# Performance work log

Hardware: AMD Instinct MI355X
Metric: run time of the kernel (lower is better)

Reference implementation:

```python
import jax, jax.numpy as jnp
import numpy as np

B, CIN, H, W = 4, 1024, 64, 64
PLANES = 256
K = 3
DIL = 2
PAD = DIL * (K - 1) // 2  # = 2
EPS = 1e-5


def setup_inputs() -> dict:
    key = jax.random.key(0)
    ks = jax.random.split(key, 16)
    d = {}
    d['x'] = jax.random.normal(ks[0], (B, CIN, H, W), dtype=jnp.float32)
    # conv1: 1x1, inplanes->planes, no bias
    d['w1'] = jax.random.normal(ks[1], (PLANES, CIN), dtype=jnp.float32) * 0.02
    d['gamma1'] = jnp.ones((PLANES,), jnp.float32)
    d['beta1'] = jnp.zeros((PLANES,), jnp.float32)
    d['mean1'] = jax.random.normal(ks[2], (PLANES,), dtype=jnp.float32) * 0.1
    d['var1'] = jax.random.uniform(ks[3], (PLANES,), minval=0.5, maxval=1.5, dtype=jnp.float32)
    # deform_offset: 3x3 conv planes->18, with bias
    d['woff'] = jax.random.normal(ks[4], (18, PLANES, K, K), dtype=jnp.float32) * 0.01
    d['boff'] = jnp.zeros((18,), jnp.float32)
    # conv2 (deformable): 3x3 planes->planes, with bias
    d['w2'] = jax.random.normal(ks[5], (PLANES, PLANES, K, K), dtype=jnp.float32) * 0.02
    d['bconv2'] = jnp.zeros((PLANES,), jnp.float32)
    d['gamma2'] = jnp.ones((PLANES,), jnp.float32)
    d['beta2'] = jnp.zeros((PLANES,), jnp.float32)
    d['mean2'] = jax.random.normal(ks[6], (PLANES,), dtype=jnp.float32) * 0.1
    d['var2'] = jax.random.uniform(ks[7], (PLANES,), minval=0.5, maxval=1.5, dtype=jnp.float32)
    # conv3: 1x1 planes->planes*4, no bias
    d['w3'] = jax.random.normal(ks[8], (PLANES * 4, PLANES), dtype=jnp.float32) * 0.02
    d['gamma3'] = jnp.ones((PLANES * 4,), jnp.float32)
    d['beta3'] = jnp.zeros((PLANES * 4,), jnp.float32)
    d['mean3'] = jax.random.normal(ks[9], (PLANES * 4,), dtype=jnp.float32) * 0.1
    d['var3'] = jax.random.uniform(ks[10], (PLANES * 4,), minval=0.5, maxval=1.5, dtype=jnp.float32)
    return d


def _bn(x, gamma, beta, mean, var):
    # inference-mode BatchNorm over channel dim (NCHW)
    inv = jax.lax.rsqrt(var + EPS)
    return (x - mean[:, None, None]) * (inv * gamma)[:, None, None] + beta[:, None, None]


def _deform_conv(x, offset, w, b):
    # x: [B,C,H,W]; offset: [B,18,H,W] ordered (dy,dx) per kernel tap; w: [O,C,3,3]
    Bn, C, Hh, Ww = x.shape
    off = offset.reshape(Bn, K * K, 2, Hh, Ww)
    off_y, off_x = off[:, :, 0], off[:, :, 1]          # [B,9,H,W]
    kk = jnp.arange(K * K)
    base_y = (kk // K) * DIL - PAD                      # [9]
    base_x = (kk % K) * DIL - PAD
    ys = jnp.arange(Hh, dtype=x.dtype)
    xs = jnp.arange(Ww, dtype=x.dtype)
    py = base_y.astype(x.dtype)[None, :, None, None] + ys[None, None, :, None] + off_y
    px = base_x.astype(x.dtype)[None, :, None, None] + xs[None, None, None, :] + off_x

    def sample_one(img, py1, px1):
        # img [C,H,W]; py1/px1 [9,H,W] -> [C,9,H,W] bilinear with zero padding
        y0 = jnp.floor(py1)
        x0 = jnp.floor(px1)
        wy = py1 - y0
        wx = px1 - x0

        def gather(yc, xc):
            yi = yc.astype(jnp.int32)
            xi = xc.astype(jnp.int32)
            valid = ((yi >= 0) & (yi < Hh) & (xi >= 0) & (xi < Ww)).astype(img.dtype)
            yi = jnp.clip(yi, 0, Hh - 1)
            xi = jnp.clip(xi, 0, Ww - 1)
            return img[:, yi, xi] * valid[None]

        v00 = gather(y0, x0)
        v01 = gather(y0, x0 + 1)
        v10 = gather(y0 + 1, x0)
        v11 = gather(y0 + 1, x0 + 1)
        return (v00 * ((1 - wy) * (1 - wx))[None] + v01 * ((1 - wy) * wx)[None]
                + v10 * (wy * (1 - wx))[None] + v11 * (wy * wx)[None])

    sampled = jax.vmap(sample_one)(x, py, px)           # [B,C,9,H,W]
    out = jnp.einsum('bckhw,ock->bohw', sampled, w.reshape(w.shape[0], C, K * K))
    return out + b[None, :, None, None]


def reference(x, w1, gamma1, beta1, mean1, var1, woff, boff, w2, bconv2,
              gamma2, beta2, mean2, var2, w3, gamma3, beta3, mean3, var3):
    residual = x
    out = jnp.einsum('bchw,oc->bohw', x, w1)            # conv1 1x1
    out = jax.nn.relu(_bn(out, gamma1, beta1, mean1, var1))
    offset = jax.lax.conv_general_dilated(
        out, woff, window_strides=(1, 1), padding=((PAD, PAD), (PAD, PAD)),
        rhs_dilation=(DIL, DIL), dimension_numbers=('NCHW', 'OIHW', 'NCHW'))
    offset = offset + boff[None, :, None, None]
    out = _deform_conv(out, offset, w2, bconv2)
    out = jax.nn.relu(_bn(out, gamma2, beta2, mean2, var2))
    out = jnp.einsum('bchw,oc->bohw', out, w3)          # conv3 1x1
    out = _bn(out, gamma3, beta3, mean3, var3)
    return jax.nn.relu(out + residual)
```

## Files before the change

kernel.cpp:

```cpp
#include <hip/hip_runtime.h>

#define EPS_BN 1e-5f

typedef __bf16 bf16x8 __attribute__((ext_vector_type(8)));
typedef float f32x4 __attribute__((ext_vector_type(4)));

__device__ __forceinline__ unsigned short f2bf(float f) {
  union { float f; unsigned u; } v; v.f = f;
  unsigned r = v.u + 0x7fffu + ((v.u >> 16) & 1u);
  return (unsigned short)(r >> 16);
}
__device__ __forceinline__ float bf2f(unsigned short h) {
  union { unsigned u; float f; } v; v.u = ((unsigned)h) << 16;
  return v.f;
}

__global__ __launch_bounds__(256) void prep_all(
    const float* __restrict__ w1, const float* __restrict__ w2, const float* __restrict__ woff,
    const float* __restrict__ w3,
    const float* g1, const float* b1, const float* m1, const float* v1,
    const float* g2, const float* b2, const float* m2, const float* v2, const float* bconv2,
    const float* g3, const float* b3, const float* m3, const float* v3,
    unsigned short* __restrict__ w1b, unsigned short* __restrict__ w2r,
    uint4* __restrict__ act1Pz, unsigned short* __restrict__ wob,
    unsigned short* __restrict__ w3b, float* __restrict__ shift3,
    float* s1, float* h1, float* s2, float* h2) {
  int bid = blockIdx.x, tid = threadIdx.x;
  if (bid < 1024) {
    int i = bid * 256 + tid;
    w1b[i] = f2bf(w1[i]);
  } else if (bid < 3328) {
    int i = (bid - 1024) * 256 + tid;
    int o = i / 2304, r = i % 2304;
    int kk = r / 256, c = r % 256;
    w2r[i] = f2bf(w2[(size_t)o * 2304 + c * 9 + kk]);
  } else if (bid < 3592) {
    int i = (bid - 3328) * 256 + tid;
    int cell = i >> 5, q = i & 31;
    int b = cell / 528, r = cell - b * 528;
    int row, col;
    if (r < 136) { row = r / 68; col = r % 68; }
    else if (r < 272) { int rr = r - 136; row = 66 + rr / 68; col = rr % 68; }
    else { int rr = r - 272; row = 2 + (rr >> 2); int c4 = rr & 3; col = (c4 < 2) ? c4 : c4 + 64; }
    act1Pz[(((size_t)(b * 68) + row) * 68 + col) * 32 + q] = uint4{0, 0, 0, 0};
  } else if (bid < 3880) {
    int i = (bid - 3592) * 256 + tid;
    int o = i / 2304, r = i % 2304;
    int kk = r / 256, c = r % 256;
    wob[i] = (o < 18) ? f2bf(woff[(size_t)o * 2304 + c * 9 + kk]) : (unsigned short)0;
  } else if (bid < 4904) {
    int i = (bid - 3880) * 256 + tid;
    int o = i >> 8;
    float sc = rsqrtf(v3[o] + EPS_BN) * g3[o];
    w3b[i] = f2bf(w3[i] * sc);
  } else if (bid < 4908) {
    int c = (bid - 4904) * 256 + tid;
    float sc = rsqrtf(v3[c] + EPS_BN) * g3[c];
    shift3[c] = b3[c] - m3[c] * sc;
  } else {
    int c = tid;
    float sc1 = rsqrtf(v1[c] + EPS_BN) * g1[c];
    s1[c] = sc1; h1[c] = b1[c] - m1[c] * sc1;
    float sc2 = rsqrtf(v2[c] + EPS_BN) * g2[c];
    s2[c] = sc2; h2[c] = b2[c] + (bconv2[c] - m2[c]) * sc2;
  }
}

__global__ __launch_bounds__(256) void gemm1_x(
    const float* __restrict__ x, const unsigned short* __restrict__ Bm,
    unsigned short* __restrict__ part, int KH) {
  __shared__ __align__(16) char blob[16896];
  __shared__ __align__(16) unsigned short sA1[4096];
  __shared__ __align__(16) unsigned short sB1[4096];
  unsigned short* sA0 = (unsigned short*)blob;
  unsigned short* sB0 = (unsigned short*)(blob + 8192);
  float* tbuf = (float*)blob;
  int tid = threadIdx.x, lane = tid & 63, wv = tid >> 6;
  int z = blockIdx.z;
  int m0 = blockIdx.y * 128, n0 = blockIdx.x * 128;
  f32x4 acc[4][4] = {};
  int rowB = tid >> 2;
  int kcolBs = (((tid & 3) ^ (rowB & 3))) * 8;
  int px = tid & 127, chalf = tid >> 7;
  int s0w = (chalf * 2) ^ (px & 3), s1w = (chalf * 2 + 1) ^ (px & 3);
  int bb = m0 >> 12, p0 = m0 & 4095;
  const float* xa = x + (size_t)bb * 4194304 + (size_t)(chalf * 16) * 4096 + (p0 + px);
  int wm = wv & 1, wn = wv >> 1;
  int lane15 = lane & 15, quad = lane >> 4, l3 = lane & 3;

  float va[16];

#define G1_ISSUE_A(K0)                                                                    \
  {                                                                                       \
    const float* xp = xa + (size_t)(K0) * 4096;                                           \
    _Pragma("unroll") for (int j = 0; j < 16; ++j) va[j] = xp[(size_t)j * 4096];          \
  }

#define G1_ISSUE_B(DB, K0)                                                                \
  {                                                                                       \
    _Pragma("unroll") for (int r = 0; r < 2; ++r) {                                       \
      const unsigned short* gp = Bm + (size_t)(n0 + r * 64 + rowB) * 1024 + (K0) + kcolBs;\
      __builtin_amdgcn_global_load_lds((const __attribute__((address_space(1))) void*)gp, \
          (__attribute__((address_space(3))) void*)&(DB)[r * 2048 + wv * 512], 16, 0, 0); \
    }                                                                                     \
  }

#define G1_CVT_WRITE(DA)                                                                  \
  {                                                                                       \
    unsigned o8[8];                                                                       \
    _Pragma("unroll") for (int j = 0; j < 8; ++j)                                         \
      o8[j] = (unsigned)f2bf(va[2 * j]) | ((unsigned)f2bf(va[2 * j + 1]) << 16);          \
    *(uint4*)((DA) + px * 32 + s0w * 8) = uint4{o8[0], o8[1], o8[2], o8[3]};              \
    *(uint4*)((DA) + px * 32 + s1w * 8) = uint4{o8[4], o8[5], o8[6], o8[7]};              \
  }

#define G1_COMPUTE(DA, DB)                                                                \
  {                                                                                       \
    bf16x8 afr[4], bfr[4];                                                                \
    _Pragma("unroll") for (int mi = 0; mi < 4; ++mi)                                      \
      afr[mi] = *(const bf16x8*)&(DA)[(wm * 64 + mi * 16 + lane15) * 32 + (quad ^ l3) * 8]; \
    _Pragma("unroll") for (int ni = 0; ni < 4; ++ni)                                      \
      bfr[ni] = *(const bf16x8*)&(DB)[(wn * 64 + ni * 16 + lane15) * 32 + (quad ^ l3) * 8]; \
    _Pragma("unroll") for (int mi = 0; mi < 4; ++mi)                                      \
      _Pragma("unroll") for (int ni = 0; ni < 4; ++ni)                                    \
        acc[mi][ni] =                                                                     \
            __builtin_amdgcn_mfma_f32_16x16x32_bf16(afr[mi], bfr[ni], acc[mi][ni], 0, 0, 0); \
  }

#define G1_BODY(K0, AC, BC, AN, BN_)                                                      \
  {                                                                                       \
    G1_ISSUE_A(K0);                                                                       \
    G1_ISSUE_B(BN_, K0);                                                                  \
    asm volatile("s_waitcnt vmcnt(18)" ::: "memory");                                     \
    asm volatile("s_waitcnt lgkmcnt(0)" ::: "memory");                                    \
    __builtin_amdgcn_s_barrier();                                                         \
    G1_COMPUTE(AC, BC);                                                                   \
    asm volatile("s_waitcnt vmcnt(2)" ::: "memory");                                      \
    G1_CVT_WRITE(AN);                                                                     \
    __builtin_amdgcn_s_barrier();                                                         \
  }

  int kbase = z * KH;
  int nst = KH >> 5;
  G1_ISSUE_A(kbase);
  G1_ISSUE_B(sB0, kbase);
  asm volatile("s_waitcnt vmcnt(2)" ::: "memory");
  G1_CVT_WRITE(sA0);
  for (int t = 0; t + 2 < nst; t += 2) {
    G1_BODY(kbase + (t + 1) * 32, sA0, sB0, sA1, sB1);
    G1_BODY(kbase + (t + 2) * 32, sA1, sB1, sA0, sB0);
  }
  G1_BODY(kbase + (nst - 1) * 32, sA0, sB0, sA1, sB1);
  asm volatile("s_waitcnt vmcnt(0)" ::: "memory");
  asm volatile("s_waitcnt lgkmcnt(0)" ::: "memory");
  __builtin_amdgcn_s_barrier();
  G1_COMPUTE(sA1, sB1);
#undef G1_ISSUE_A
#undef G1_ISSUE_B
#undef G1_CVT_WRITE
#undef G1_COMPUTE
#undef G1_BODY

  unsigned short* outH = part + (size_t)z * 16384 * 256;
  int trow = tid >> 3;
  int tcol16 = (tid & 7) * 16;
  int growBase = m0 + (trow >> 4) * 64 + (trow & 15);
#pragma unroll
  for (int mi = 0; mi < 4; ++mi) {
    __syncthreads();
#pragma unroll
    for (int ni = 0; ni < 4; ++ni)
#pragma unroll
      for (int reg = 0; reg < 4; ++reg)
        tbuf[(wm * 16 + quad * 4 + reg) * 132 + wn * 64 + ni * 16 + lane15] = acc[mi][ni][reg];
    __syncthreads();
    int gr = growBase + mi * 16;
    const float* lp = &tbuf[trow * 132 + tcol16];
    unsigned o[8];
#pragma unroll
    for (int j = 0; j < 8; ++j)
      o[j] = (unsigned)f2bf(lp[2 * j]) | ((unsigned)f2bf(lp[2 * j + 1]) << 16);
    unsigned short* op = outH + (size_t)gr * 256 + n0 + tcol16;
    *(uint4*)(op) = uint4{o[0], o[1], o[2], o[3]};
    *(uint4*)(op + 8) = uint4{o[4], o[5], o[6], o[7]};
  }
}

__global__ __launch_bounds__(256) void gemm_split(
    const unsigned short* __restrict__ A, const unsigned short* __restrict__ Bm,
    unsigned short* __restrict__ part, int M, int N, int K, int KH) {
  __shared__ __align__(16) char blob[32768];
  __shared__ __align__(16) unsigned short sA1[8192];
  __shared__ __align__(16) unsigned short sB1[8192];
  unsigned short* sA0 = (unsigned short*)blob;
  unsigned short* sB0 = (unsigned short*)(blob + 16384);
  float* tbuf = (float*)blob;
  int tid = threadIdx.x, lane = tid & 63, wv = tid >> 6;
  int z = blockIdx.z;
  int m0 = blockIdx.y * 128, n0 = blockIdx.x * 128;
  f32x4 acc[4][4] = {};
  int rowS = tid >> 3;
  int colS = (((tid & 7) ^ (rowS & 7))) * 8;
  int wm = wv & 1, wn = wv >> 1;
  int lane15 = lane & 15, quad = lane >> 4, l7 = lane & 7;

#define GS_STAGE(dA, dB, K0)                                                              \
  {                                                                                       \
    int k0_ = (K0);                                                                       \
    _Pragma("unroll") for (int r = 0; r < 4; ++r) {                                       \
      const unsigned short* gp = A + (size_t)(m0 + r * 32 + rowS) * K + k0_ + colS;       \
      __builtin_amdgcn_global_load_lds((const __attribute__((address_space(1))) void*)gp, \
          (__attribute__((address_space(3))) void*)&(dA)[r * 2048 + wv * 512], 16, 0, 0); \
    }                                                                                     \
    _Pragma("unroll") for (int r = 0; r < 4; ++r) {                                       \
      const unsigned short* gp = Bm + (size_t)(n0 + r * 32 + rowS) * K + k0_ + colS;      \
      __builtin_amdgcn_global_load_lds((const __attribute__((address_space(1))) void*)gp, \
          (__attribute__((address_space(3))) void*)&(dB)[r * 2048 + wv * 512], 16, 0, 0); \
    }                                                                                     \
  }

#define GS_COMPUTE(dA, dB)                                                                \
  {                                                                                       \
    _Pragma("unroll") for (int kq = 0; kq < 2; ++kq) {                                    \
      bf16x8 afr[4], bfr[4];                                                              \
      _Pragma("unroll") for (int mi = 0; mi < 4; ++mi)                                    \
        afr[mi] = *(const bf16x8*)&(dA)[(wm * 64 + mi * 16 + lane15) * 64 +               \
                                        ((kq * 4 + quad) ^ l7) * 8];                      \
      _Pragma("unroll") for (int ni = 0; ni < 4; ++ni)                                    \
        bfr[ni] = *(const bf16x8*)&(dB)[(wn * 64 + ni * 16 + lane15) * 64 +               \
                                        ((kq * 4 + quad) ^ l7) * 8];                      \
      _Pragma("unroll") for (int mi = 0; mi < 4; ++mi)                                    \
        _Pragma("unroll") for (int ni = 0; ni < 4; ++ni)                                  \
          acc[mi][ni] =                                                                   \
              __builtin_amdgcn_mfma_f32_16x16x32_bf16(afr[mi], bfr[ni], acc[mi][ni], 0, 0, 0); \
    }                                                                                     \
  }

  int kbase = z * KH;
  int nst = KH >> 6;
  GS_STAGE(sA0, sB0, kbase);
  for (int t = 0; t < nst; t += 2) {
    GS_STAGE(sA1, sB1, kbase + (t + 1) * 64);
    asm volatile("s_waitcnt vmcnt(8)" ::: "memory");
    __builtin_amdgcn_s_barrier();
    GS_COMPUTE(sA0, sB0);
    __builtin_amdgcn_s_barrier();
    if (t + 2 < nst) {
      GS_STAGE(sA0, sB0, kbase + (t + 2) * 64);
      asm volatile("s_waitcnt vmcnt(8)" ::: "memory");
    } else {
      asm volatile("s_waitcnt vmcnt(0)" ::: "memory");
    }
    __builtin_amdgcn_s_barrier();
    GS_COMPUTE(sA1, sB1);
    __builtin_amdgcn_s_barrier();
  }
#undef GS_STAGE
#undef GS_COMPUTE

  unsigned short* outH = part + (size_t)z * M * N;
  int trow = tid >> 3;
  int tcol16 = (tid & 7) * 16;
  int growBase = m0 + (trow >> 4) * 64 + (trow & 15);
#pragma unroll
  for (int mi = 0; mi < 4; ++mi) {
    __syncthreads();
#pragma unroll
    for (int ni = 0; ni < 4; ++ni)
#pragma unroll
      for (int reg = 0; reg < 4; ++reg)
        tbuf[(wm * 16 + quad * 4 + reg) * 132 + wn * 64 + ni * 16 + lane15] = acc[mi][ni][reg];
    __syncthreads();
    int gr = growBase + mi * 16;
    const float* lp = &tbuf[trow * 132 + tcol16];
    unsigned o[8];
#pragma unroll
    for (int j = 0; j < 8; ++j)
      o[j] = (unsigned)f2bf(lp[2 * j]) | ((unsigned)f2bf(lp[2 * j + 1]) << 16);
    unsigned short* op = outH + (size_t)gr * 256 + n0 + tcol16;
    *(uint4*)(op) = uint4{o[0], o[1], o[2], o[3]};
    *(uint4*)(op + 8) = uint4{o[4], o[5], o[6], o[7]};
  }
}

template <int NS, int PAD>
__global__ __launch_bounds__(256) void epi_bn(const unsigned short* __restrict__ part,
                                              const float* __restrict__ scale,
                                              const float* __restrict__ shift,
                                              unsigned short* __restrict__ outT,
                                              unsigned short* __restrict__ outP) {
  int gid = blockIdx.x * 256 + threadIdx.x;
  int row = gid >> 5, c0 = (gid & 31) * 8;
  float v[8] = {};
#pragma unroll
  for (int s = 0; s < NS; ++s) {
    uint4 q = *(const uint4*)(part + (size_t)s * 16384 * 256 + (size_t)row * 256 + c0);
    unsigned u[4] = {q.x, q.y, q.z, q.w};
#pragma unroll
    for (int j = 0; j < 4; ++j) {
      v[2 * j]     += bf2f((unsigned short)(u[j] & 0xffffu));
      v[2 * j + 1] += bf2f((unsigned short)(u[j] >> 16));
    }
  }
  float sc[8], sh[8];
  *(float4*)&sc[0] = *(const float4*)(scale + c0); *(float4*)&sc[4] = *(const float4*)(scale + c0 + 4);
  *(float4*)&sh[0] = *(const float4*)(shift + c0); *(float4*)&sh[4] = *(const float4*)(shift + c0 + 4);
  unsigned o[4];
#pragma unroll
  for (int j = 0; j < 4; ++j) {
    float lo = fmaxf(v[2 * j] * sc[2 * j] + sh[2 * j], 0.f);
    float hi = fmaxf(v[2 * j + 1] * sc[2 * j + 1] + sh[2 * j + 1], 0.f);
    o[j] = (unsigned)f2bf(lo) | ((unsigned)f2bf(hi) << 16);
  }
  uint4 pk{o[0], o[1], o[2], o[3]};
  *(uint4*)(outT + (size_t)row * 256 + c0) = pk;
  if constexpr (PAD) {
    int bb = row >> 12, p = row & 4095;
    *(uint4*)(outP + (((size_t)(bb * 68) + (p >> 6) + 2) * 68 + (p & 63) + 2) * 256 + c0) = pk;
  }
}

__global__ __launch_bounds__(256) void gemm_res(
    const unsigned short* __restrict__ A, const unsigned short* __restrict__ Bm,
    float* __restrict__ outp, const float* __restrict__ shift3,
    const float* __restrict__ resid, int M, int N, int K, long bStrideB, long bStrideOut) {
  __shared__ __align__(16) char blob[16896];
  __shared__ __align__(16) unsigned short sA1[4096];
  __shared__ __align__(16) unsigned short sB1[4096];
  unsigned short* sA0 = (unsigned short*)blob;
  unsigned short* sB0 = (unsigned short*)(blob + 8192);
  float* tbuf = (float*)blob;
  int tid = threadIdx.x, lane = tid & 63, wv = tid >> 6;
  int z = blockIdx.z;
  const unsigned short* Bz = Bm + (size_t)z * bStrideB;
  int m0 = blockIdx.y * 128, n0 = blockIdx.x * 128;
  f32x4 acc[4][4] = {};
  int rowA = tid >> 2;
  int kcolS = (((tid & 3) ^ (rowA & 3))) * 8;
  int wm = wv & 1, wn = wv >> 1;
  int lane15 = lane & 15, quad = lane >> 4, l3 = lane & 3;

#define GR_STAGE(dA, dB, K0)                                                              \
  {                                                                                       \
    int k0_ = (K0);                                                                       \
    _Pragma("unroll") for (int r = 0; r < 2; ++r) {                                       \
      const unsigned short* gp = A + (size_t)(m0 + r * 64 + rowA) * K + k0_ + kcolS;      \
      __builtin_amdgcn_global_load_lds((const __attribute__((address_space(1))) void*)gp, \
          (__attribute__((address_space(3))) void*)&(dA)[r * 2048 + wv * 512], 16, 0, 0); \
    }                                                                                     \
    _Pragma("unroll") for (int r = 0; r < 2; ++r) {                                       \
      const unsigned short* gp = Bz + (size_t)(n0 + r * 64 + rowA) * K + k0_ + kcolS;     \
      __builtin_amdgcn_global_load_lds((const __attribute__((address_space(1))) void*)gp, \
          (__attribute__((address_space(3))) void*)&(dB)[r * 2048 + wv * 512], 16, 0, 0); \
    }                                                                                     \
  }

#define GR_COMPUTE(dA, dB)                                                                \
  {                                                                                       \
    bf16x8 afr[4], bfr[4];                                                                \
    _Pragma("unroll") for (int mi = 0; mi < 4; ++mi)                                      \
      afr[mi] = *(const bf16x8*)&(dA)[(wm * 64 + mi * 16 + lane15) * 32 + (quad ^ l3) * 8]; \
    _Pragma("unroll") for (int ni = 0; ni < 4; ++ni)                                      \
      bfr[ni] = *(const bf16x8*)&(dB)[(wn * 64 + ni * 16 + lane15) * 32 + (quad ^ l3) * 8]; \
    _Pragma("unroll") for (int mi = 0; mi < 4; ++mi)                                      \
      _Pragma("unroll") for (int ni = 0; ni < 4; ++ni)                                    \
        acc[mi][ni] =                                                                     \
            __builtin_amdgcn_mfma_f32_16x16x32_bf16(afr[mi], bfr[ni], acc[mi][ni], 0, 0, 0); \
  }

  int nst = K >> 5;
  GR_STAGE(sA0, sB0, 0);
  for (int t = 0; t < nst; t += 2) {
    GR_STAGE(sA1, sB1, (t + 1) * 32);
    asm volatile("s_waitcnt vmcnt(4)" ::: "memory");
    __builtin_amdgcn_s_barrier();
    GR_COMPUTE(sA0, sB0);
    __builtin_amdgcn_s_barrier();
    if (t + 2 < nst) {
      GR_STAGE(sA0, sB0, (t + 2) * 32);
      asm volatile("s_waitcnt vmcnt(4)" ::: "memory");
    } else {
      asm volatile("s_waitcnt vmcnt(0)" ::: "memory");
    }
    __builtin_amdgcn_s_barrier();
    GR_COMPUTE(sA1, sB1);
    __builtin_amdgcn_s_barrier();
  }
#undef GR_STAGE
#undef GR_COMPUTE

  float* outF = outp + (size_t)z * bStrideOut;
  const float* res = resid + (size_t)z * bStrideOut;
  int trow = tid >> 3;
  int tcol = (tid & 7) * 4;
  int growBase = m0 + (trow >> 4) * 64 + (trow & 15);
#pragma unroll
  for (int mi = 0; mi < 4; ++mi) {
    __syncthreads();
#pragma unroll
    for (int ni = 0; ni < 4; ++ni)
#pragma unroll
      for (int reg = 0; reg < 4; ++reg)
        tbuf[(wm * 16 + quad * 4 + reg) * 132 + wn * 64 + ni * 16 + lane15] = acc[mi][ni][reg];
    __syncthreads();
    int gr = growBase + mi * 16;
    float sh = shift3[gr];
    const float* rp = res + (size_t)gr * N + n0 + tcol;
    float* op = outF + (size_t)gr * N + n0 + tcol;
    const float* lp = &tbuf[trow * 132 + tcol];
#pragma unroll
    for (int j = 0; j < 4; ++j) {
      float4 rv = *(const float4*)(rp + j * 32);
      float4 lv = *(const float4*)(lp + j * 32);
      float4 ov;
      ov.x = fmaxf(lv.x + sh + rv.x, 0.f);
      ov.y = fmaxf(lv.y + sh + rv.y, 0.f);
      ov.z = fmaxf(lv.z + sh + rv.z, 0.f);
      ov.w = fmaxf(lv.w + sh + rv.w, 0.f);
      *(float4*)(op + j * 32) = ov;
    }
  }
}

__global__ __launch_bounds__(256) void off_gemm(const unsigned short* __restrict__ actP,
                                                const unsigned short* __restrict__ wob,
                                                const float* __restrict__ boff,
                                                float* __restrict__ offsP) {
  __shared__ __align__(16) unsigned short sA0[4096];
  __shared__ __align__(16) unsigned short sA1[4096];
  __shared__ __align__(16) unsigned short sA2[4096];
  __shared__ __align__(16) unsigned short sA3[4096];
  __shared__ __align__(16) unsigned short sB0[2048];
  __shared__ __align__(16) unsigned short sB1[2048];
  __shared__ __align__(16) unsigned short sB2[2048];
  __shared__ __align__(16) unsigned short sB3[2048];
  int tid = threadIdx.x, lane = tid & 63, wv = tid >> 6;
  int m0 = blockIdx.x * 64;
  int lane15 = lane & 15, quad8 = (lane >> 4) * 8;
  int rowA = tid >> 3;
  int kc = (tid & 7) * 8;

  const unsigned short* baseA[2];
#pragma unroll
  for (int r = 0; r < 2; ++r) {
    int row = m0 + r * 32 + rowA;
    int b = row >> 12, p = row & 4095;
    baseA[r] = actP + (((size_t)(b * 68) + (p >> 6) + 2) * 68 + (p & 63) + 2) * 256 + kc;
  }
  const unsigned short* baseB = wob + (size_t)rowA * 2304 + kc;

  f32x4 acc[2] = {};

#define OG_STAGE(dA, dB, S)                                                               \
  {                                                                                       \
    int s_ = (S); int kk_ = s_ >> 2; int c0_ = (s_ & 3) * 64;                             \
    long shift_ = (long)(((kk_ / 3) * 2 - 2) * 68 + ((kk_ % 3) * 2 - 2));                 \
    _Pragma("unroll") for (int r = 0; r < 2; ++r) {                                       \
      const unsigned short* gp = baseA[r] + shift_ * 256 + c0_;                           \
      __builtin_amdgcn_global_load_lds((const __attribute__((address_space(1))) void*)gp, \
          (__attribute__((address_space(3))) void*)&(dA)[r * 2048 + wv * 512], 16, 0, 0); \
    }                                                                                     \
    {                                                                                     \
      const unsigned short* gp = baseB + kk_ * 256 + c0_;                                 \
      __builtin_amdgcn_global_load_lds((const __attribute__((address_space(1))) void*)gp, \
          (__attribute__((address_space(3))) void*)&(dB)[wv * 512], 16, 0, 0);            \
    }                                                                                     \
  }

#define OG_COMPUTE(dA, dB)                                                                \
  {                                                                                       \
    bf16x8 afr[2], bfr[2][2];                                                             \
    _Pragma("unroll") for (int kq = 0; kq < 2; ++kq) {                                    \
      afr[kq] = *(const bf16x8*)&(dA)[(wv * 16 + lane15) * 64 + kq * 32 + quad8];         \
      _Pragma("unroll") for (int ni = 0; ni < 2; ++ni)                                    \
        bfr[kq][ni] = *(const bf16x8*)&(dB)[(ni * 16 + lane15) * 64 + kq * 32 + quad8];   \
    }                                                                                     \
    _Pragma("unroll") for (int kq = 0; kq < 2; ++kq)                                      \
      _Pragma("unroll") for (int ni = 0; ni < 2; ++ni)                                    \
        acc[ni] = __builtin_amdgcn_mfma_f32_16x16x32_bf16(afr[kq], bfr[kq][ni], acc[ni], 0, 0, 0); \
  }

#define OG_STEP6(AC, BC, SN, AN, BN_)                                                     \
  {                                                                                       \
    OG_STAGE(AN, BN_, SN);                                                                \
    asm volatile("s_waitcnt vmcnt(6)" ::: "memory");                                      \
    __builtin_amdgcn_s_barrier();                                                         \
    OG_COMPUTE(AC, BC);                                                                   \
    __builtin_amdgcn_s_barrier();                                                         \
  }

  OG_STAGE(sA0, sB0, 0);
  OG_STAGE(sA1, sB1, 1);
  for (int s4 = 0; s4 < 32; s4 += 4) {
    OG_STEP6(sA0, sB0, s4 + 2, sA2, sB2);
    OG_STEP6(sA1, sB1, s4 + 3, sA3, sB3);
    OG_STEP6(sA2, sB2, s4 + 4, sA0, sB0);
    OG_STEP6(sA3, sB3, s4 + 5, sA1, sB1);
  }
  OG_STEP6(sA0, sB0, 34, sA2, sB2);
  OG_STEP6(sA1, sB1, 35, sA3, sB3);
  asm volatile("s_waitcnt vmcnt(3)" ::: "memory");
  __builtin_amdgcn_s_barrier();
  OG_COMPUTE(sA2, sB2);
  __builtin_amdgcn_s_barrier();
  asm volatile("s_waitcnt vmcnt(0)" ::: "memory");
  __builtin_amdgcn_s_barrier();
  OG_COMPUTE(sA3, sB3);
#undef OG_STAGE
#undef OG_COMPUTE
#undef OG_STEP6

#pragma unroll
  for (int ni = 0; ni < 2; ++ni) {
    int o = ni * 16 + lane15;
    if (o < 18) {
      float bo = boff[o];
#pragma unroll
      for (int reg = 0; reg < 4; ++reg) {
        int row = m0 + wv * 16 + (lane >> 4) * 4 + reg;
        offsP[(size_t)row * 18 + o] = acc[ni][reg] + bo;
      }
    }
  }
}

__global__ __launch_bounds__(256) void deform_sample(const unsigned short* __restrict__ act1T,
                                                     const float* __restrict__ offsP,
                                                     unsigned short* __restrict__ S) {
  int g = threadIdx.x >> 5, t = threadIdx.x & 31;
  int idx = blockIdx.x * 8 + g;
  int b = idx >> 12, p = idx & 4095;
  int h = p >> 6, w = p & 63;
  const unsigned short* actb = act1T + (size_t)b * 4096 * 256 + t * 8;
  unsigned short* Sp = S + (size_t)idx * 2304 + t * 8;
  float ov = (t < 18) ? offsP[(size_t)idx * 18 + t] : 0.f;
#pragma unroll
  for (int kk = 0; kk < 9; ++kk) {
    float offy = __shfl(ov, 2 * kk, 32);
    float offx = __shfl(ov, 2 * kk + 1, 32);
    float py = (float)(h + (kk / 3) * 2 - 2) + offy;
    float px = (float)(w + (kk % 3) * 2 - 2) + offx;
    float fy = floorf(py), fx = floorf(px);
    int y0 = (int)fy, x0 = (int)fx;
    float wy = py - fy, wx = px - fx;
    bool yv0 = (y0 >= 0 && y0 < 64), yv1 = (y0 >= -1 && y0 < 63);
    bool xv0 = (x0 >= 0 && x0 < 64), xv1 = (x0 >= -1 && x0 < 63);
    const unsigned short* cb = actb + (y0 * 64 + x0) * 256;
    uint4 q00{0,0,0,0}, q01{0,0,0,0}, q10{0,0,0,0}, q11{0,0,0,0};
    if (yv0 && xv0) q00 = *(const uint4*)(cb);
    if (yv0 && xv1) q01 = *(const uint4*)(cb + 256);
    if (yv1 && xv0) q10 = *(const uint4*)(cb + 64 * 256);
    if (yv1 && xv1) q11 = *(const uint4*)(cb + 64 * 256 + 256);
    float w00 = (1.f - wy) * (1.f - wx), w01 = (1.f - wy) * wx;
    float w10 = wy * (1.f - wx), w11 = wy * wx;
    unsigned u00[4] = {q00.x, q00.y, q00.z, q00.w};
    unsigned u01[4] = {q01.x, q01.y, q01.z, q01.w};
    unsigned u10[4] = {q10.x, q10.y, q10.z, q10.w};
    unsigned u11[4] = {q11.x, q11.y, q11.z, q11.w};
    unsigned out[4];
#pragma unroll
    for (int j = 0; j < 4; ++j) {
      float lo = bf2f((unsigned short)(u00[j] & 0xffffu)) * w00 +
                 bf2f((unsigned short)(u01[j] & 0xffffu)) * w01 +
                 bf2f((unsigned short)(u10[j] & 0xffffu)) * w10 +
                 bf2f((unsigned short)(u11[j] & 0xffffu)) * w11;
      float hi = bf2f((unsigned short)(u00[j] >> 16)) * w00 +
                 bf2f((unsigned short)(u01[j] >> 16)) * w01 +
                 bf2f((unsigned short)(u10[j] >> 16)) * w10 +
                 bf2f((unsigned short)(u11[j] >> 16)) * w11;
      out[j] = (unsigned)f2bf(lo) | ((unsigned)f2bf(hi) << 16);
    }
    *(uint4*)(Sp + kk * 256) = uint4{out[0], out[1], out[2], out[3]};
  }
}

extern "C" void kernel_launch(void* const* d_in, const int* in_sizes, int n_in,
                              void* d_out, int out_size, void* d_ws, size_t ws_size,
                              hipStream_t stream) {
  const float* x      = (const float*)d_in[0];
  const float* w1     = (const float*)d_in[1];
  const float* gamma1 = (const float*)d_in[2];
  const float* beta1  = (const float*)d_in[3];
  const float* mean1  = (const float*)d_in[4];
  const float* var1   = (const float*)d_in[5];
  const float* woff   = (const float*)d_in[6];
  const float* boff   = (const float*)d_in[7];
  const float* w2     = (const float*)d_in[8];
  const float* bconv2 = (const float*)d_in[9];
  const float* gamma2 = (const float*)d_in[10];
  const float* beta2  = (const float*)d_in[11];
  const float* mean2  = (const float*)d_in[12];
  const float* var2   = (const float*)d_in[13];
  const float* w3     = (const float*)d_in[14];
  const float* gamma3 = (const float*)d_in[15];
  const float* beta3  = (const float*)d_in[16];
  const float* mean3  = (const float*)d_in[17];
  const float* var3   = (const float*)d_in[18];

  char* ws = (char*)d_ws;
  unsigned short* act1T = (unsigned short*)(ws + 33554432);
  unsigned short* act2T = (unsigned short*)(ws + 41943040);
  unsigned short* S     = (unsigned short*)(ws + 50331648);
  float*          offs  = (float*)(ws + 125829120);
  unsigned short* w1b   = (unsigned short*)(ws + 127008768);
  unsigned short* w2r   = (unsigned short*)(ws + 127533056);
  unsigned short* w3b   = (unsigned short*)(ws + 128712704);
  float*          bnS1  = (float*)(ws + 129236992);
  float*          bnH1  = (float*)(ws + 129238016);
  float*          bnS2  = (float*)(ws + 129239040);
  float*          bnH2  = (float*)(ws + 129240064);
  float*          shift3= (float*)(ws + 129241088);
  unsigned short* act1P = S;
  unsigned short* part1 = (unsigned short*)(ws + 62914560);
  unsigned short* part2 = (unsigned short*)ws;
  unsigned short* wob   = act2T;

  prep_all<<<4909, 256, 0, stream>>>(w1, w2, woff, w3,
                                     gamma1, beta1, mean1, var1,
                                     gamma2, beta2, mean2, var2, bconv2,
                                     gamma3, beta3, mean3, var3,
                                     w1b, w2r, (uint4*)act1P, wob, w3b, shift3,
                                     bnS1, bnH1, bnS2, bnH2);

  gemm1_x<<<dim3(2, 128, 2), 256, 0, stream>>>(x, w1b, part1, 512);
  epi_bn<2, 1><<<2048, 256, 0, stream>>>(part1, bnS1, bnH1, act1T, act1P);

  off_gemm<<<256, 256, 0, stream>>>(act1P, wob, boff, offs);
  deform_sample<<<dim3(2048), 256, 0, stream>>>(act1T, offs, S);

  gemm_split<<<dim3(2, 128, 2), 256, 0, stream>>>(S, w2r, part2, 16384, 256, 2304, 1152);
  epi_bn<2, 0><<<2048, 256, 0, stream>>>(part2, bnS2, bnH2, act2T, nullptr);

  gemm_res<<<dim3(32, 8, 4), 256, 0, stream>>>(w3b, act2T, (float*)d_out, shift3, x,
                                               1024, 4096, 256, 4096L * 256, 4194304L);
}
```

Before: 267.0 us.

## Drop split-K in conv1 and deform GEMMs, fuse BN+ReLU epilogue into them

The conv1 and deformable-conv GEMMs no longer split K across two z-slices and write bf16 partials. Each now uses 64x128 tiles over the full K range and applies BN scale/shift plus ReLU directly in its epilogue, so the two epi_bn kernels go away. This removes the partial-sum write/read round trip and two launches, and keeps the same block count by halving the M tile. In exchange each block runs a longer K loop with a smaller tile, so there is less data reuse per block. Partials are no longer rounded to bf16 before being summed.

```diff
diff --git a/kernel.cpp b/kernel.cpp
--- a/kernel.cpp
+++ b/kernel.cpp
@@ -68,32 +68,32 @@
 
 __global__ __launch_bounds__(256) void gemm1_x(
     const float* __restrict__ x, const unsigned short* __restrict__ Bm,
-    unsigned short* __restrict__ part, int KH) {
+    const float* __restrict__ scale, const float* __restrict__ shift,
+    unsigned short* __restrict__ outT, unsigned short* __restrict__ outP) {
   __shared__ __align__(16) char blob[16896];
-  __shared__ __align__(16) unsigned short sA1[4096];
+  __shared__ __align__(16) unsigned short sA1[2048];
   __shared__ __align__(16) unsigned short sB1[4096];
   unsigned short* sA0 = (unsigned short*)blob;
-  unsigned short* sB0 = (unsigned short*)(blob + 8192);
+  unsigned short* sB0 = (unsigned short*)(blob + 4096);
   float* tbuf = (float*)blob;
   int tid = threadIdx.x, lane = tid & 63, wv = tid >> 6;
-  int z = blockIdx.z;
-  int m0 = blockIdx.y * 128, n0 = blockIdx.x * 128;
-  f32x4 acc[4][4] = {};
+  int m0 = blockIdx.y * 64, n0 = blockIdx.x * 128;
+  f32x4 acc[2][4] = {};
   int rowB = tid >> 2;
-  int kcolBs = (((tid & 3) ^ (rowB & 3))) * 8;
-  int px = tid & 127, chalf = tid >> 7;
-  int s0w = (chalf * 2) ^ (px & 3), s1w = (chalf * 2 + 1) ^ (px & 3);
+  int kcolBs = ((tid & 3) ^ (rowB & 3)) * 8;
+  int px = tid & 63;
+  int sw = wv ^ (px & 3);
   int bb = m0 >> 12, p0 = m0 & 4095;
-  const float* xa = x + (size_t)bb * 4194304 + (size_t)(chalf * 16) * 4096 + (p0 + px);
+  const float* xa = x + (size_t)bb * 4194304 + (size_t)(wv * 8) * 4096 + (p0 + px);
   int wm = wv & 1, wn = wv >> 1;
   int lane15 = lane & 15, quad = lane >> 4, l3 = lane & 3;
 
-  float va[16];
+  float va[8];
 
 #define G1_ISSUE_A(K0)                                                                    \
   {                                                                                       \
     const float* xp = xa + (size_t)(K0) * 4096;                                           \
-    _Pragma("unroll") for (int j = 0; j < 16; ++j) va[j] = xp[(size_t)j * 4096];          \
+    _Pragma("unroll") for (int j = 0; j < 8; ++j) va[j] = xp[(size_t)j * 4096];           \
   }
 
 #define G1_ISSUE_B(DB, K0)                                                                \
@@ -107,21 +107,20 @@
 
 #define G1_CVT_WRITE(DA)                                                                  \
   {                                                                                       \
-    unsigned o8[8];                                                                       \
-    _Pragma("unroll") for (int j = 0; j < 8; ++j)                                         \
-      o8[j] = (unsigned)f2bf(va[2 * j]) | ((unsigned)f2bf(va[2 * j + 1]) << 16);          \
-    *(uint4*)((DA) + px * 32 + s0w * 8) = uint4{o8[0], o8[1], o8[2], o8[3]};              \
-    *(uint4*)((DA) + px * 32 + s1w * 8) = uint4{o8[4], o8[5], o8[6], o8[7]};              \
+    unsigned o4[4];                                                                       \
+    _Pragma("unroll") for (int j = 0; j < 4; ++j)                                         \
+      o4[j] = (unsigned)f2bf(va[2 * j]) | ((unsigned)f2bf(va[2 * j + 1]) << 16);          \
+    *(uint4*)((DA) + px * 32 + sw * 8) = uint4{o4[0], o4[1], o4[2], o4[3]};               \
   }
 
 #define G1_COMPUTE(DA, DB)                                                                \
   {                                                                                       \
-    bf16x8 afr[4], bfr[4];                                                                \
-    _Pragma("unroll") for (int mi = 0; mi < 4; ++mi)                                      \
-      afr[mi] = *(const bf16x8*)&(DA)[(wm * 64 + mi * 16 + lane15) * 32 + (quad ^ l3) * 8]; \
+    bf16x8 afr[2], bfr[4];                                                                \
+    _Pragma("unroll") for (int mi = 0; mi < 2; ++mi)                                      \
+      afr[mi] = *(const bf16x8*)&(DA)[(wm * 32 + mi * 16 + lane15) * 32 + (quad ^ l3) * 8]; \
     _Pragma("unroll") for (int ni = 0; ni < 4; ++ni)                                      \
       bfr[ni] = *(const bf16x8*)&(DB)[(wn * 64 + ni * 16 + lane15) * 32 + (quad ^ l3) * 8]; \
-    _Pragma("unroll") for (int mi = 0; mi < 4; ++mi)                                      \
+    _Pragma("unroll") for (int mi = 0; mi < 2; ++mi)                                      \
       _Pragma("unroll") for (int ni = 0; ni < 4; ++ni)                                    \
         acc[mi][ni] =                                                                     \
             __builtin_amdgcn_mfma_f32_16x16x32_bf16(afr[mi], bfr[ni], acc[mi][ni], 0, 0, 0); \
@@ -131,7 +130,7 @@
   {                                                                                       \
     G1_ISSUE_A(K0);                                                                       \
     G1_ISSUE_B(BN_, K0);                                                                  \
-    asm volatile("s_waitcnt vmcnt(18)" ::: "memory");                                     \
+    asm volatile("s_waitcnt vmcnt(10)" ::: "memory");                                     \
     asm volatile("s_waitcnt lgkmcnt(0)" ::: "memory");                                    \
     __builtin_amdgcn_s_barrier();                                                         \
     G1_COMPUTE(AC, BC);                                                                   \
@@ -140,17 +139,16 @@
     __builtin_amdgcn_s_barrier();                                                         \
   }
 
-  int kbase = z * KH;
-  int nst = KH >> 5;
-  G1_ISSUE_A(kbase);
-  G1_ISSUE_B(sB0, kbase);
+  const int nst = 32;
+  G1_ISSUE_A(0);
+  G1_ISSUE_B(sB0, 0);
   asm volatile("s_waitcnt vmcnt(2)" ::: "memory");
   G1_CVT_WRITE(sA0);
   for (int t = 0; t + 2 < nst; t += 2) {
-    G1_BODY(kbase + (t + 1) * 32, sA0, sB0, sA1, sB1);
-    G1_BODY(kbase + (t + 2) * 32, sA1, sB1, sA0, sB0);
-  }
-  G1_BODY(kbase + (nst - 1) * 32, sA0, sB0, sA1, sB1);
+    G1_BODY((t + 1) * 32, sA0, sB0, sA1, sB1);
+    G1_BODY((t + 2) * 32, sA1, sB1, sA0, sB0);
+  }
+  G1_BODY((nst - 1) * 32, sA0, sB0, sA1, sB1);
   asm volatile("s_waitcnt vmcnt(0)" ::: "memory");
   asm volatile("s_waitcnt lgkmcnt(0)" ::: "memory");
   __builtin_amdgcn_s_barrier();
@@ -161,12 +159,17 @@
 #undef G1_COMPUTE
 #undef G1_BODY
 
-  unsigned short* outH = part + (size_t)z * 16384 * 256;
   int trow = tid >> 3;
   int tcol16 = (tid & 7) * 16;
-  int growBase = m0 + (trow >> 4) * 64 + (trow & 15);
-#pragma unroll
-  for (int mi = 0; mi < 4; ++mi) {
+  int c0 = n0 + tcol16;
+  float sc[16], sh[16];
+#pragma unroll
+  for (int q = 0; q < 4; ++q) {
+    *(float4*)&sc[q * 4] = *(const float4*)(scale + c0 + q * 4);
+    *(float4*)&sh[q * 4] = *(const float4*)(shift + c0 + q * 4);
+  }
+#pragma unroll
+  for (int mi = 0; mi < 2; ++mi) {
     __syncthreads();
 #pragma unroll
     for (int ni = 0; ni < 4; ++ni)
@@ -174,96 +177,104 @@
       for (int reg = 0; reg < 4; ++reg)
         tbuf[(wm * 16 + quad * 4 + reg) * 132 + wn * 64 + ni * 16 + lane15] = acc[mi][ni][reg];
     __syncthreads();
-    int gr = growBase + mi * 16;
+    int gr = m0 + (trow >> 4) * 32 + (trow & 15) + mi * 16;
     const float* lp = &tbuf[trow * 132 + tcol16];
     unsigned o[8];
 #pragma unroll
-    for (int j = 0; j < 8; ++j)
-      o[j] = (unsigned)f2bf(lp[2 * j]) | ((unsigned)f2bf(lp[2 * j + 1]) << 16);
-    unsigned short* op = outH + (size_t)gr * 256 + n0 + tcol16;
-    *(uint4*)(op) = uint4{o[0], o[1], o[2], o[3]};
-    *(uint4*)(op + 8) = uint4{o[4], o[5], o[6], o[7]};
-  }
-}
-
-__global__ __launch_bounds__(256) void gemm_split(
+    for (int j = 0; j < 8; ++j) {
+      float lo = fmaxf(lp[2 * j] * sc[2 * j] + sh[2 * j], 0.f);
+      float hi = fmaxf(lp[2 * j + 1] * sc[2 * j + 1] + sh[2 * j + 1], 0.f);
+      o[j] = (unsigned)f2bf(lo) | ((unsigned)f2bf(hi) << 16);
+    }
+    uint4 pk0{o[0], o[1], o[2], o[3]}, pk1{o[4], o[5], o[6], o[7]};
+    unsigned short* op = outT + (size_t)gr * 256 + c0;
+    *(uint4*)(op) = pk0;
+    *(uint4*)(op + 8) = pk1;
+    int b2 = gr >> 12, p = gr & 4095;
+    unsigned short* pp = outP + (((size_t)(b2 * 68) + (p >> 6) + 2) * 68 + (p & 63) + 2) * 256 + c0;
+    *(uint4*)(pp) = pk0;
+    *(uint4*)(pp + 8) = pk1;
+  }
+}
+
+__global__ __launch_bounds__(256) void gemm2(
     const unsigned short* __restrict__ A, const unsigned short* __restrict__ Bm,
-    unsigned short* __restrict__ part, int M, int N, int K, int KH) {
-  __shared__ __align__(16) char blob[32768];
-  __shared__ __align__(16) unsigned short sA1[8192];
-  __shared__ __align__(16) unsigned short sB1[8192];
+    const float* __restrict__ scale, const float* __restrict__ shift,
+    unsigned short* __restrict__ outT) {
+  __shared__ __align__(16) char blob[16896];
+  __shared__ __align__(16) unsigned short sA1[2048];
+  __shared__ __align__(16) unsigned short sB1[4096];
   unsigned short* sA0 = (unsigned short*)blob;
-  unsigned short* sB0 = (unsigned short*)(blob + 16384);
+  unsigned short* sB0 = (unsigned short*)(blob + 4096);
   float* tbuf = (float*)blob;
   int tid = threadIdx.x, lane = tid & 63, wv = tid >> 6;
-  int z = blockIdx.z;
-  int m0 = blockIdx.y * 128, n0 = blockIdx.x * 128;
-  f32x4 acc[4][4] = {};
-  int rowS = tid >> 3;
-  int colS = (((tid & 7) ^ (rowS & 7))) * 8;
+  int m0 = blockIdx.y * 64, n0 = blockIdx.x * 128;
+  f32x4 acc[2][4] = {};
+  int rowS = tid >> 2;
+  int kcolS = ((tid & 3) ^ (rowS & 3)) * 8;
   int wm = wv & 1, wn = wv >> 1;
-  int lane15 = lane & 15, quad = lane >> 4, l7 = lane & 7;
-
-#define GS_STAGE(dA, dB, K0)                                                              \
+  int lane15 = lane & 15, quad = lane >> 4, l3 = lane & 3;
+
+#define G2_STAGE(dA, dB, K0)                                                              \
   {                                                                                       \
     int k0_ = (K0);                                                                       \
-    _Pragma("unroll") for (int r = 0; r < 4; ++r) {                                       \
-      const unsigned short* gp = A + (size_t)(m0 + r * 32 + rowS) * K + k0_ + colS;       \
+    {                                                                                     \
+      const unsigned short* gp = A + (size_t)(m0 + rowS) * 2304 + k0_ + kcolS;            \
       __builtin_amdgcn_global_load_lds((const __attribute__((address_space(1))) void*)gp, \
-          (__attribute__((address_space(3))) void*)&(dA)[r * 2048 + wv * 512], 16, 0, 0); \
-    }                                                                                     \
-    _Pragma("unroll") for (int r = 0; r < 4; ++r) {                                       \
-      const unsigned short* gp = Bm + (size_t)(n0 + r * 32 + rowS) * K + k0_ + colS;      \
+          (__attribute__((address_space(3))) void*)&(dA)[wv * 512], 16, 0, 0);            \
+    }                                                                                     \
+    _Pragma("unroll") for (int r = 0; r < 2; ++r) {                                       \
+      const unsigned short* gp = Bm + (size_t)(n0 + r * 64 + rowS) * 2304 + k0_ + kcolS;  \
       __builtin_amdgcn_global_load_lds((const __attribute__((address_space(1))) void*)gp, \
           (__attribute__((address_space(3))) void*)&(dB)[r * 2048 + wv * 512], 16, 0, 0); \
     }                                                                                     \
   }
 
-#define GS_COMPUTE(dA, dB)                                                                \
-  {                                                                                       \
-    _Pragma("unroll") for (int kq = 0; kq < 2; ++kq) {                                    \
-      bf16x8 afr[4], bfr[4];                                                              \
-      _Pragma("unroll") for (int mi = 0; mi < 4; ++mi)                                    \
-        afr[mi] = *(const bf16x8*)&(dA)[(wm * 64 + mi * 16 + lane15) * 64 +               \
-                                        ((kq * 4 + quad) ^ l7) * 8];                      \
+#define G2_COMPUTE(dA, dB)                                                                \
+  {                                                                                       \
+    bf16x8 afr[2], bfr[4];                                                                \
+    _Pragma("unroll") for (int mi = 0; mi < 2; ++mi)                                      \
+      afr[mi] = *(const bf16x8*)&(dA)[(wm * 32 + mi * 16 + lane15) * 32 + (quad ^ l3) * 8]; \
+    _Pragma("unroll") for (int ni = 0; ni < 4; ++ni)                                      \
+      bfr[ni] = *(const bf16x8*)&(dB)[(wn * 64 + ni * 16 + lane15) * 32 + (quad ^ l3) * 8]; \
+    _Pragma("unroll") for (int mi = 0; mi < 2; ++mi)                                      \
       _Pragma("unroll") for (int ni = 0; ni < 4; ++ni)                                    \
-        bfr[ni] = *(const bf16x8*)&(dB)[(wn * 64 + ni * 16 + lane15) * 64 +               \
-                                        ((kq * 4 + quad) ^ l7) * 8];                      \
-      _Pragma("unroll") for (int mi = 0; mi < 4; ++mi)                                    \
-        _Pragma("unroll") for (int ni = 0; ni < 4; ++ni)                                  \
-          acc[mi][ni] =                                                                   \
-              __builtin_amdgcn_mfma_f32_16x16x32_bf16(afr[mi], bfr[ni], acc[mi][ni], 0, 0, 0); \
-    }                                                                                     \
-  }
-
-  int kbase = z * KH;
-  int nst = KH >> 6;
-  GS_STAGE(sA0, sB0, kbase);
+        acc[mi][ni] =                                                                     \
+            __builtin_amdgcn_mfma_f32_16x16x32_bf16(afr[mi], bfr[ni], acc[mi][ni], 0, 0, 0); \
+  }
+
+  const int nst = 72;
+  G2_STAGE(sA0, sB0, 0);
   for (int t = 0; t < nst; t += 2) {
-    GS_STAGE(sA1, sB1, kbase + (t + 1) * 64);
-    asm volatile("s_waitcnt vmcnt(8)" ::: "memory");
-    __builtin_amdgcn_s_barrier();
-    GS_COMPUTE(sA0, sB0);
+    G2_STAGE(sA1, sB1, (t + 1) * 32);
+    asm volatile("s_waitcnt vmcnt(3)" ::: "memory");
+    __builtin_amdgcn_s_barrier();
+    G2_COMPUTE(sA0, sB0);
     __builtin_amdgcn_s_barrier();
     if (t + 2 < nst) {
-      GS_STAGE(sA0, sB0, kbase + (t + 2) * 64);
-      asm volatile("s_waitcnt vmcnt(8)" ::: "memory");
+      G2_STAGE(sA0, sB0, (t + 2) * 32);
+      asm volatile("s_waitcnt vmcnt(3)" ::: "memory");
     } else {
       asm volatile("s_waitcnt vmcnt(0)" ::: "memory");
     }
     __builtin_amdgcn_s_barrier();
-    GS_COMPUTE(sA1, sB1);
-    __builtin_amdgcn_s_barrier();
-  }
-#undef GS_STAGE
-#undef GS_COMPUTE
-
-  unsigned short* outH = part + (size_t)z * M * N;
+    G2_COMPUTE(sA1, sB1);
+    __builtin_amdgcn_s_barrier();
+  }
+#undef G2_STAGE
+#undef G2_COMPUTE
+
   int trow = tid >> 3;
   int tcol16 = (tid & 7) * 16;
-  int growBase = m0 + (trow >> 4) * 64 + (trow & 15);
-#pragma unroll
-  for (int mi = 0; mi < 4; ++mi) {
+  int c0 = n0 + tcol16;
+  float sc[16], sh[16];
+#pragma unroll
+  for (int q = 0; q < 4; ++q) {
+    *(float4*)&sc[q * 4] = *(const float4*)(scale + c0 + q * 4);
+    *(float4*)&sh[q * 4] = *(const float4*)(shift + c0 + q * 4);
+  }
+#pragma unroll
+  for (int mi = 0; mi < 2; ++mi) {
     __syncthreads();
 #pragma unroll
     for (int ni = 0; ni < 4; ++ni)
@@ -271,52 +282,18 @@
       for (int reg = 0; reg < 4; ++reg)
         tbuf[(wm * 16 + quad * 4 + reg) * 132 + wn * 64 + ni * 16 + lane15] = acc[mi][ni][reg];
     __syncthreads();
-    int gr = growBase + mi * 16;
+    int gr = m0 + (trow >> 4) * 32 + (trow & 15) + mi * 16;
     const float* lp = &tbuf[trow * 132 + tcol16];
     unsigned o[8];
 #pragma unroll
-    for (int j = 0; j < 8; ++j)
-      o[j] = (unsigned)f2bf(lp[2 * j]) | ((unsigned)f2bf(lp[2 * j + 1]) << 16);
-    unsigned short* op = outH + (size_t)gr * 256 + n0 + tcol16;
+    for (int j = 0; j < 8; ++j) {
+      float lo = fmaxf(lp[2 * j] * sc[2 * j] + sh[2 * j], 0.f);
+      float hi = fmaxf(lp[2 * j + 1] * sc[2 * j + 1] + sh[2 * j + 1], 0.f);
+      o[j] = (unsigned)f2bf(lo) | ((unsigned)f2bf(hi) << 16);
+    }
+    unsigned short* op = outT + (size_t)gr * 256 + c0;
     *(uint4*)(op) = uint4{o[0], o[1], o[2], o[3]};
     *(uint4*)(op + 8) = uint4{o[4], o[5], o[6], o[7]};
-  }
-}
-
-template <int NS, int PAD>
-__global__ __launch_bounds__(256) void epi_bn(const unsigned short* __restrict__ part,
-                                              const float* __restrict__ scale,
-                                              const float* __restrict__ shift,
-                                              unsigned short* __restrict__ outT,
-                                              unsigned short* __restrict__ outP) {
-  int gid = blockIdx.x * 256 + threadIdx.x;
-  int row = gid >> 5, c0 = (gid & 31) * 8;
-  float v[8] = {};
-#pragma unroll
-  for (int s = 0; s < NS; ++s) {
-    uint4 q = *(const uint4*)(part + (size_t)s * 16384 * 256 + (size_t)row * 256 + c0);
-    unsigned u[4] = {q.x, q.y, q.z, q.w};
-#pragma unroll
-    for (int j = 0; j < 4; ++j) {
-      v[2 * j]     += bf2f((unsigned short)(u[j] & 0xffffu));
-      v[2 * j + 1] += bf2f((unsigned short)(u[j] >> 16));
-    }
-  }
-  float sc[8], sh[8];
-  *(float4*)&sc[0] = *(const float4*)(scale + c0); *(float4*)&sc[4] = *(const float4*)(scale + c0 + 4);
-  *(float4*)&sh[0] = *(const float4*)(shift + c0); *(float4*)&sh[4] = *(const float4*)(shift + c0 + 4);
-  unsigned o[4];
-#pragma unroll
-  for (int j = 0; j < 4; ++j) {
-    float lo = fmaxf(v[2 * j] * sc[2 * j] + sh[2 * j], 0.f);
-    float hi = fmaxf(v[2 * j + 1] * sc[2 * j + 1] + sh[2 * j + 1], 0.f);
-    o[j] = (unsigned)f2bf(lo) | ((unsigned)f2bf(hi) << 16);
-  }
-  uint4 pk{o[0], o[1], o[2], o[3]};
-  *(uint4*)(outT + (size_t)row * 256 + c0) = pk;
-  if constexpr (PAD) {
-    int bb = row >> 12, p = row & 4095;
-    *(uint4*)(outP + (((size_t)(bb * 68) + (p >> 6) + 2) * 68 + (p & 63) + 2) * 256 + c0) = pk;
   }
 }
 
@@ -611,8 +588,6 @@
   float*          bnH2  = (float*)(ws + 129240064);
   float*          shift3= (float*)(ws + 129241088);
   unsigned short* act1P = S;
-  unsigned short* part1 = (unsigned short*)(ws + 62914560);
-  unsigned short* part2 = (unsigned short*)ws;
   unsigned short* wob   = act2T;
 
   prep_all<<<4909, 256, 0, stream>>>(w1, w2, woff, w3,
@@ -622,14 +597,12 @@
                                      w1b, w2r, (uint4*)act1P, wob, w3b, shift3,
                                      bnS1, bnH1, bnS2, bnH2);
 
-  gemm1_x<<<dim3(2, 128, 2), 256, 0, stream>>>(x, w1b, part1, 512);
-  epi_bn<2, 1><<<2048, 256, 0, stream>>>(part1, bnS1, bnH1, act1T, act1P);
+  gemm1_x<<<dim3(2, 256), 256, 0, stream>>>(x, w1b, bnS1, bnH1, act1T, act1P);
 
   off_gemm<<<256, 256, 0, stream>>>(act1P, wob, boff, offs);
   deform_sample<<<dim3(2048), 256, 0, stream>>>(act1T, offs, S);
 
-  gemm_split<<<dim3(2, 128, 2), 256, 0, stream>>>(S, w2r, part2, 16384, 256, 2304, 1152);
-  epi_bn<2, 0><<<2048, 256, 0, stream>>>(part2, bnS2, bnH2, act2T, nullptr);
+  gemm2<<<dim3(2, 256), 256, 0, stream>>>(S, w2r, bnS2, bnH2, act2T);
 
   gemm_res<<<dim3(32, 8, 4), 256, 0, stream>>>(w3b, act2T, (float*)d_out, shift3, x,
                                                1024, 4096, 256, 4096L * 256, 4194304L);
```

Result: slower. 273.7 us (+2.5%).

## Use four-stage K=32 LDS pipeline in split-K GEMM instead of double buffering

Applied to the files above, without the earlier changes.

The split-K GEMM kernel now uses K-tiles of 32 instead of 64 and four LDS buffers in a rotating pipeline, replacing the previous two-buffer scheme. The staging layout and XOR swizzle are adapted to 32-wide rows, and each compute step issues one k-slice of MFMAs. The goal is deeper prefetch so more global loads are in flight per compute step, hiding latency. The cost is twice as many barriers per unit of K, and the larger total LDS footprint may reduce occupancy.

```diff
diff --git a/kernel.cpp b/kernel.cpp
--- a/kernel.cpp
+++ b/kernel.cpp
@@ -189,31 +189,35 @@
 __global__ __launch_bounds__(256) void gemm_split(
     const unsigned short* __restrict__ A, const unsigned short* __restrict__ Bm,
     unsigned short* __restrict__ part, int M, int N, int K, int KH) {
-  __shared__ __align__(16) char blob[32768];
-  __shared__ __align__(16) unsigned short sA1[8192];
-  __shared__ __align__(16) unsigned short sB1[8192];
+  __shared__ __align__(16) char blob[16896];
+  __shared__ __align__(16) unsigned short sA1[4096];
+  __shared__ __align__(16) unsigned short sB1[4096];
+  __shared__ __align__(16) unsigned short sA2[4096];
+  __shared__ __align__(16) unsigned short sB2[4096];
+  __shared__ __align__(16) unsigned short sA3[4096];
+  __shared__ __align__(16) unsigned short sB3[4096];
   unsigned short* sA0 = (unsigned short*)blob;
-  unsigned short* sB0 = (unsigned short*)(blob + 16384);
+  unsigned short* sB0 = (unsigned short*)(blob + 8192);
   float* tbuf = (float*)blob;
   int tid = threadIdx.x, lane = tid & 63, wv = tid >> 6;
   int z = blockIdx.z;
   int m0 = blockIdx.y * 128, n0 = blockIdx.x * 128;
   f32x4 acc[4][4] = {};
-  int rowS = tid >> 3;
-  int colS = (((tid & 7) ^ (rowS & 7))) * 8;
+  int rowA = tid >> 2;
+  int kcolS = (((tid & 3) ^ (rowA & 3))) * 8;
   int wm = wv & 1, wn = wv >> 1;
-  int lane15 = lane & 15, quad = lane >> 4, l7 = lane & 7;
+  int lane15 = lane & 15, quad = lane >> 4, l3 = lane & 3;
 
 #define GS_STAGE(dA, dB, K0)                                                              \
   {                                                                                       \
     int k0_ = (K0);                                                                       \
-    _Pragma("unroll") for (int r = 0; r < 4; ++r) {                                       \
-      const unsigned short* gp = A + (size_t)(m0 + r * 32 + rowS) * K + k0_ + colS;       \
+    _Pragma("unroll") for (int r = 0; r < 2; ++r) {                                       \
+      const unsigned short* gp = A + (size_t)(m0 + r * 64 + rowA) * K + k0_ + kcolS;      \
       __builtin_amdgcn_global_load_lds((const __attribute__((address_space(1))) void*)gp, \
           (__attribute__((address_space(3))) void*)&(dA)[r * 2048 + wv * 512], 16, 0, 0); \
     }                                                                                     \
-    _Pragma("unroll") for (int r = 0; r < 4; ++r) {                                       \
-      const unsigned short* gp = Bm + (size_t)(n0 + r * 32 + rowS) * K + k0_ + colS;      \
+    _Pragma("unroll") for (int r = 0; r < 2; ++r) {                                       \
+      const unsigned short* gp = Bm + (size_t)(n0 + r * 64 + rowA) * K + k0_ + kcolS;     \
       __builtin_amdgcn_global_load_lds((const __attribute__((address_space(1))) void*)gp, \
           (__attribute__((address_space(3))) void*)&(dB)[r * 2048 + wv * 512], 16, 0, 0); \
     }                                                                                     \
@@ -221,42 +225,49 @@
 
 #define GS_COMPUTE(dA, dB)                                                                \
   {                                                                                       \
-    _Pragma("unroll") for (int kq = 0; kq < 2; ++kq) {                                    \
-      bf16x8 afr[4], bfr[4];                                                              \
-      _Pragma("unroll") for (int mi = 0; mi < 4; ++mi)                                    \
-        afr[mi] = *(const bf16x8*)&(dA)[(wm * 64 + mi * 16 + lane15) * 64 +               \
-                                        ((kq * 4 + quad) ^ l7) * 8];                      \
+    bf16x8 afr[4], bfr[4];                                                                \
+    _Pragma("unroll") for (int mi = 0; mi < 4; ++mi)                                      \
+      afr[mi] = *(const bf16x8*)&(dA)[(wm * 64 + mi * 16 + lane15) * 32 + (quad ^ l3) * 8]; \
+    _Pragma("unroll") for (int ni = 0; ni < 4; ++ni)                                      \
+      bfr[ni] = *(const bf16x8*)&(dB)[(wn * 64 + ni * 16 + lane15) * 32 + (quad ^ l3) * 8]; \
+    _Pragma("unroll") for (int mi = 0; mi < 4; ++mi)                                      \
       _Pragma("unroll") for (int ni = 0; ni < 4; ++ni)                                    \
-        bfr[ni] = *(const bf16x8*)&(dB)[(wn * 64 + ni * 16 + lane15) * 64 +               \
-                                        ((kq * 4 + quad) ^ l7) * 8];                      \
-      _Pragma("unroll") for (int mi = 0; mi < 4; ++mi)                                    \
-        _Pragma("unroll") for (int ni = 0; ni < 4; ++ni)                                  \
-          acc[mi][ni] =                                                                   \
-              __builtin_amdgcn_mfma_f32_16x16x32_bf16(afr[mi], bfr[ni], acc[mi][ni], 0, 0, 0); \
-    }                                                                                     \
+        acc[mi][ni] =                                                                     \
+            __builtin_amdgcn_mfma_f32_16x16x32_bf16(afr[mi], bfr[ni], acc[mi][ni], 0, 0, 0); \
+  }
+
+#define GS_STEP8(AC, BC, SN, AN, BN_)                                                     \
+  {                                                                                       \
+    GS_STAGE(AN, BN_, kbase + (SN) * 32);                                                 \
+    asm volatile("s_waitcnt vmcnt(8)" ::: "memory");                                      \
+    __builtin_amdgcn_s_barrier();                                                         \
+    GS_COMPUTE(AC, BC);                                                                   \
+    __builtin_amdgcn_s_barrier();                                                         \
   }
 
   int kbase = z * KH;
-  int nst = KH >> 6;
+  int nst = KH >> 5;
   GS_STAGE(sA0, sB0, kbase);
-  for (int t = 0; t < nst; t += 2) {
-    GS_STAGE(sA1, sB1, kbase + (t + 1) * 64);
-    asm volatile("s_waitcnt vmcnt(8)" ::: "memory");
-    __builtin_amdgcn_s_barrier();
-    GS_COMPUTE(sA0, sB0);
-    __builtin_amdgcn_s_barrier();
-    if (t + 2 < nst) {
-      GS_STAGE(sA0, sB0, kbase + (t + 2) * 64);
-      asm volatile("s_waitcnt vmcnt(8)" ::: "memory");
-    } else {
-      asm volatile("s_waitcnt vmcnt(0)" ::: "memory");
-    }
-    __builtin_amdgcn_s_barrier();
-    GS_COMPUTE(sA1, sB1);
-    __builtin_amdgcn_s_barrier();
-  }
+  GS_STAGE(sA1, sB1, kbase + 32);
+  for (int s4 = 0; s4 < nst - 4; s4 += 4) {
+    GS_STEP8(sA0, sB0, s4 + 2, sA2, sB2);
+    GS_STEP8(sA1, sB1, s4 + 3, sA3, sB3);
+    GS_STEP8(sA2, sB2, s4 + 4, sA0, sB0);
+    GS_STEP8(sA3, sB3, s4 + 5, sA1, sB1);
+  }
+  GS_STEP8(sA0, sB0, nst - 2, sA2, sB2);
+  GS_STEP8(sA1, sB1, nst - 1, sA3, sB3);
+  asm volatile("s_waitcnt vmcnt(4)" ::: "memory");
+  __builtin_amdgcn_s_barrier();
+  GS_COMPUTE(sA2, sB2);
+  __builtin_amdgcn_s_barrier();
+  asm volatile("s_waitcnt vmcnt(0)" ::: "memory");
+  __builtin_amdgcn_s_barrier();
+  GS_COMPUTE(sA3, sB3);
+  __builtin_amdgcn_s_barrier();
 #undef GS_STAGE
 #undef GS_COMPUTE
+#undef GS_STEP8
 
   unsigned short* outH = part + (size_t)z * M * N;
   int trow = tid >> 3;
@@ -486,7 +497,7 @@
     asm volatile("s_waitcnt vmcnt(6)" ::: "memory");                                      \
     __builtin_amdgcn_s_barrier();                                                         \
     OG_COMPUTE(AC, BC);                                                                   \
-    __builtin_amdgcn_s_barrier();                                                         \
+    __builtin_amdgcn_s_barrier();                                                        \
   }
 
   OG_STAGE(sA0, sB0, 0);
```

New measurement: 270.3 us. About the same (+1.2%).
